# Kernel tuning notes

Measured on AMD Instinct MI355X. Metric: run time of the kernel, lower is better.

The kernel has to match this reference:

```python
import jax, jax.numpy as jnp
import numpy as np

B, S, DIM = 2, 4096, 768
G = DIM // 3          # gate_dim = 256
H, DK = 4, G // 4     # heads=4, d_k=64
SCALE = 1.0 / np.sqrt(DK)


def setup_inputs() -> dict:
    key = jax.random.key(0)
    ks = jax.random.split(key, 9)
    r = lambda k, shp, s: (jax.random.normal(k, shp, dtype=jnp.float32) * s)
    w_s = 1.0 / np.sqrt(G)
    return {
        "x": r(ks[0], (B, S, DIM), 1.0),
        "wq": r(ks[1], (G, G), w_s), "bq": r(ks[2], (G,), 0.01),
        "wk": r(ks[3], (G, G), w_s), "bk": r(ks[4], (G,), 0.01),
        "wv": r(ks[5], (G, G), w_s), "bv": r(ks[6], (G,), 0.01),
        "wo": r(ks[7], (G, G), w_s), "bo": r(ks[8], (G,), 0.01),
    }


def reference(x, wq, bq, wk, bk, wv, bv, wo, bo):
    # chunk(3, dim=-1): q/k/v slices of width G
    xq, xk, xv = x[..., :G], x[..., G:2 * G], x[..., 2 * G:3 * G]
    # linear projections then split into heads: [b, s, h, d]
    q = (xq @ wq.T + bq).reshape(B, S, H, DK)
    k = (xk @ wk.T + bk).reshape(B, S, H, DK)
    v = (xv @ wv.T + bv).reshape(B, S, H, DK)
    scores = jnp.einsum('bihd,bjhd->bijh', q, k) * SCALE  # [b, i, j, h]
    # NOTE: original applies Softmax(dim=1) -> over the QUERY axis i
    attn = jax.nn.softmax(scores, axis=1)
    out = jnp.einsum('bijh,bjhd->bihd', attn, v).reshape(B, S, G)
    return out @ wo.T + bo
```

## Files before the change

kernel.cpp:

```cpp
#include <hip/hip_runtime.h>

#define SEQ   4096
#define HH    4
#define SCALE 0.125f
#define SC2   0.18033688011112042f
#define C16   -23.083120654223414f

typedef __bf16 bf16x8 __attribute__((ext_vector_type(8)));
typedef __bf16 bf16x4 __attribute__((ext_vector_type(4)));
typedef float  f32x4  __attribute__((ext_vector_type(4)));

constexpr size_t OFF_W16  = 0;
constexpr size_t OFF_A    = 131072;
constexpr size_t OFF_AO   = 294912;
constexpr size_t OFF_X16  = 9732096;
constexpr size_t OFF_Q16  = 12877824;
constexpr size_t K16OFF   = 2097152;
constexpr size_t V16OFF   = 4194304;
constexpr size_t OFF_PZ   = 16023552;

__device__ __forceinline__ f32x4 mf(bf16x8 a, bf16x8 b, f32x4 c) {
    return __builtin_amdgcn_mfma_f32_16x16x32_bf16(a, b, c, 0, 0, 0);
}

__device__ __forceinline__ void gload16(const __bf16* g, __bf16* l) {
    __builtin_amdgcn_global_load_lds(
        (const __attribute__((address_space(1))) unsigned int*)g,
        (__attribute__((address_space(3))) unsigned int*)l, 16, 0, 0);
}

__device__ __forceinline__ float ex2(float x) {
    return __builtin_amdgcn_exp2f(x);
}

__global__ void k_prep(const float* __restrict__ x,
                       const float* __restrict__ wq, const float* __restrict__ wk,
                       const float* __restrict__ wv, const float* __restrict__ wo,
                       float* __restrict__ ws) {
    int bx = blockIdx.x, t = threadIdx.x;
    if (bx < 6144) {
        size_t i4 = ((size_t)bx * 256 + t) * 4;
        float4 v = *(const float4*)(x + i4);
        bf16x4 o = {(__bf16)v.x, (__bf16)v.y, (__bf16)v.z, (__bf16)v.w};
        *(bf16x4*)((__bf16*)(ws + OFF_X16) + i4) = o;
    } else if (bx < 6400) {
        int q = bx - 6144;
        int y = q >> 6;
        const float* src = (y == 0) ? wq : (y == 1) ? wk : (y == 2) ? wv : wo;
        float sc = (y == 0) ? SC2 : 1.0f;
        size_t i4 = ((size_t)(q & 63) * 256 + t) * 4;
        float4 v = *(const float4*)(src + i4);
        bf16x4 o = {(__bf16)(v.x * sc), (__bf16)(v.y * sc),
                    (__bf16)(v.z * sc), (__bf16)(v.w * sc)};
        *(bf16x4*)((__bf16*)(ws + OFF_W16) + (size_t)y * 65536 + i4) = o;
    } else {
        size_t i4 = ((size_t)(bx - 6400) * 256 + t) * 4;
        *(float4*)(ws + OFF_AO + i4) = make_float4(0.f, 0.f, 0.f, 0.f);
    }
}

__global__ __launch_bounds__(256) void k_qkv_mfma(const float* __restrict__ bq,
                                                  const float* __restrict__ bk,
                                                  const float* __restrict__ bv,
                                                  float* __restrict__ ws) {
    __shared__ __bf16 sbuf[4][2][1024];
    int t = threadIdx.x, lane = t & 63, w = t >> 6;
    int yw = blockIdx.y;
    int ntb = blockIdx.z * 8;
    int row0 = blockIdx.x * 64 + w * 16;
    int mrow = lane & 15, quad = lane >> 4;
    const __bf16* X16 = (const __bf16*)(ws + OFF_X16);
    const __bf16* W16 = (const __bf16*)(ws + OFF_W16) + (size_t)yw * 65536;
    const float* bias = (yw == 0) ? bq : (yw == 1) ? bk : bv;
    __bf16* Qb = (__bf16*)(ws + OFF_Q16);
    f32x4 acc[8];
#pragma unroll
    for (int n = 0; n < 8; n++) acc[n] = {0.f, 0.f, 0.f, 0.f};
    const __bf16* ap = X16 + (size_t)(row0 + mrow) * 768 + yw * 256 + quad * 8;
    const __bf16* bp = W16 + (size_t)ntb * 4096 + (size_t)mrow * 256 + quad * 8;
    for (int kc = 0; kc < 256; kc += 32) {
        bf16x8 a = *(const bf16x8*)(ap + kc);
#pragma unroll
        for (int nt = 0; nt < 8; nt++) {
            bf16x8 b = *(const bf16x8*)(bp + (size_t)nt * 4096 + kc);
            acc[nt] = mf(a, b, acc[nt]);
        }
    }
    int T = blockIdx.x * 4 + w;
    int b_ = T >> 8, Ts = T & 255;
    int th = Ts & 1;
#pragma unroll
    for (int nt = 0; nt < 8; nt++) {
        int hsel = nt >> 2, c4 = nt & 3;
        int n = (ntb + nt) * 16 + mrow;
        float bb = bias[n];
        if (yw == 0) bb *= SC2;
        __bf16* sb = &sbuf[w][hsel][0];
#pragma unroll
        for (int r = 0; r < 4; r++) {
            float val = acc[nt][r] + bb;
            int loff;
            if (yw == 0) {
                int q2 = ((c4 & 1) << 1) | (mrow >> 3);
                loff = (c4 >> 1) * 512 + (q2 * 16 + quad * 4 + r) * 8 + (mrow & 7);
            } else if (yw == 1) {
                int q2 = ((c4 & 1) << 1) | (mrow >> 3);
                int piece = ((quad & 1) * 2 + (c4 >> 1)) * 4 + q2;
                loff = piece * 64 + ((quad >> 1) * 4 + r) * 8 + (mrow & 7);
            } else {
                loff = c4 * 256 + (quad >> 1) * 128 + mrow * 8 + (quad & 1) * 4 + r;
            }
            sb[loff] = (__bf16)val;
        }
    }
#pragma unroll
    for (int hsel = 0; hsel < 2; hsel++) {
        int h = blockIdx.z * 2 + hsel;
        int bh = b_ * HH + h;
        const __bf16* sb = &sbuf[w][hsel][0];
#pragma unroll
        for (int rd = 0; rd < 2; rd++) {
            int g = rd * 64 + lane;
            bf16x8 vv = *(const bf16x8*)(sb + g * 8);
            size_t gaddr;
            if (yw == 0) {
                gaddr = (((size_t)bh * 256 + Ts) * 2) * 512 + (size_t)g * 8;
            } else if (yw == 1) {
                int p = g >> 3;
                gaddr = K16OFF + (((size_t)bh * 128 + (Ts >> 1)) * 4 + (p >> 2)) * 512
                        + (size_t)((p & 3) * 128 + th * 64 + (g & 7) * 8);
            } else {
                int p = g >> 4;
                gaddr = V16OFF + (((size_t)bh * 128 + (Ts >> 1)) * 4 + (p >> 1)) * 512
                        + (size_t)((th * 2 + (p & 1)) * 128 + (g & 15) * 8);
            }
            *(bf16x8*)(Qb + gaddr) = vv;
        }
    }
}

__global__ __launch_bounds__(256) void k_colstats(float* __restrict__ ws) {
    __shared__ __bf16 qbuf[2][4096];
    int t = threadIdx.x, lane = t & 63, w = t >> 6;
    int jb = blockIdx.x, iy = blockIdx.y, bh = blockIdx.z;
    int jc0 = jb * 8 + w * 2;
    const __bf16* Qp = (const __bf16*)(ws + OFF_Q16);
    const __bf16* Kp = Qp + K16OFF;
    const __bf16* kb = Kp + ((size_t)(bh * 128 + jc0) * 4) * 512 + lane * 8;
    bf16x8 kA0 = *(const bf16x8*)(kb);
    bf16x8 kA1 = *(const bf16x8*)(kb + 512);
    bf16x8 kB0 = *(const bf16x8*)(kb + 1024);
    bf16x8 kB1 = *(const bf16x8*)(kb + 1536);
    bf16x8 kC0 = *(const bf16x8*)(kb + 2048);
    bf16x8 kC1 = *(const bf16x8*)(kb + 2560);
    bf16x8 kD0 = *(const bf16x8*)(kb + 3072);
    bf16x8 kD1 = *(const bf16x8*)(kb + 3584);
    const __bf16* q0 = Qp + ((size_t)(bh * 256 + iy * 16) * 2) * 512 +
                       w * 1024 + lane * 8;
    gload16(q0, qbuf[0] + w * 1024);
    gload16(q0 + 512, qbuf[0] + w * 1024 + 512);
    __syncthreads();
    const f32x4 cin = {C16, C16, C16, C16};
    float z0 = 0.f, z1 = 0.f, z2 = 0.f, z3 = 0.f;
    for (int ic = 0; ic < 4; ic++) {
        const __bf16* cur = qbuf[ic & 1];
        if (ic < 3) {
            const __bf16* qn = Qp + ((size_t)(bh * 256 + iy * 16 + (ic + 1) * 4) * 2) * 512 +
                               w * 1024 + lane * 8;
            gload16(qn, qbuf[(ic + 1) & 1] + w * 1024);
            gload16(qn + 512, qbuf[(ic + 1) & 1] + w * 1024 + 512);
        }
#pragma unroll
        for (int it = 0; it < 4; it++) {
            bf16x8 a0 = *(const bf16x8*)(cur + it * 1024 + lane * 8);
            bf16x8 a1 = *(const bf16x8*)(cur + it * 1024 + 512 + lane * 8);
            f32x4 cA = mf(a0, kA0, cin); cA = mf(a1, kA1, cA);
            f32x4 cB = mf(a0, kB0, cin); cB = mf(a1, kB1, cB);
            f32x4 cC = mf(a0, kC0, cin); cC = mf(a1, kC1, cC);
            f32x4 cD = mf(a0, kD0, cin); cD = mf(a1, kD1, cD);
#pragma unroll
            for (int r = 0; r < 4; r++) {
                z0 += ex2(cA[r]);
                z1 += ex2(cB[r]);
                z2 += ex2(cC[r]);
                z3 += ex2(cD[r]);
            }
        }
        __syncthreads();
    }
    z0 += __shfl_xor(z0, 16, 64);
    z0 += __shfl_xor(z0, 32, 64);
    z1 += __shfl_xor(z1, 16, 64);
    z1 += __shfl_xor(z1, 32, 64);
    z2 += __shfl_xor(z2, 16, 64);
    z2 += __shfl_xor(z2, 32, 64);
    z3 += __shfl_xor(z3, 16, 64);
    z3 += __shfl_xor(z3, 32, 64);
    if (lane < 16) {
        size_t o = OFF_PZ + (size_t)iy * 32768 + (size_t)bh * SEQ +
                   jc0 * 32 + ((lane >> 2) << 3) + (lane & 3);
        ws[o] = z0;
        ws[o + 4] = z1;
        ws[o + 32] = z2;
        ws[o + 36] = z3;
    }
}

__global__ void k_afin(float* __restrict__ ws) {
    int idx = blockIdx.x * 256 + threadIdx.x;
    const float* pz = ws + OFF_PZ;
    float Z = 0.f;
#pragma unroll
    for (int y = 0; y < 16; y++) Z += pz[(size_t)y * 32768 + idx];
    ws[OFF_A + idx] = C16 - __log2f(Z);
}

__global__ __launch_bounds__(256) void k_attnpv(float* __restrict__ ws) {
    __shared__ __align__(16) char pool[28672];
    float* sA = (float*)(pool + 24576);
    int t = threadIdx.x, lane = t & 63, w = t >> 6;
    int jy = blockIdx.y, bh = blockIdx.z;
    int itp = blockIdx.x * 4 + w;
    int it0 = itp * 2;
    int mrow = lane & 15, quad = lane >> 4;
    const __bf16* Qp = (const __bf16*)(ws + OFF_Q16);
    const __bf16* Kp = Qp + K16OFF;
    const __bf16* Vp = Qp + V16OFF;

    {
        const float* Ag = ws + OFF_A + (size_t)bh * SEQ + jy * 1024;
        *(float4*)(sA + t * 4) = *(const float4*)(Ag + t * 4);
    }
    const __bf16* qb = Qp + ((size_t)(bh * 256 + it0) * 2) * 512 + lane * 8;
    bf16x8 aq00 = *(const bf16x8*)(qb);
    bf16x8 aq01 = *(const bf16x8*)(qb + 512);
    bf16x8 aq10 = *(const bf16x8*)(qb + 1024);
    bf16x8 aq11 = *(const bf16x8*)(qb + 1536);

    f32x4 oT0[4], oT1[4];
#pragma unroll
    for (int nd = 0; nd < 4; nd++) {
        oT0[nd] = {0.f, 0.f, 0.f, 0.f};
        oT1[nd] = {0.f, 0.f, 0.f, 0.f};
    }
    int c0g = jy * 32;
    const __bf16* kg = Kp + ((size_t)(bh * 128 + c0g) * 4) * 512 + w * 512 + lane * 8;
    const __bf16* vg = Vp + ((size_t)(bh * 128 + c0g) * 4) * 512 + w * 512 + lane * 8;
    gload16(kg, (__bf16*)pool + w * 512);
    gload16(vg, (__bf16*)(pool + 4096) + w * 512);
    kg += 2048; vg += 2048;
    __syncthreads();

    int bc = 0;
    for (int jt = 0; jt < 32; ++jt) {
        int bn = (bc == 2) ? 0 : bc + 1;
        if (jt < 31) {
            gload16(kg, (__bf16*)(pool + bn * 8192) + w * 512);
            gload16(vg, (__bf16*)(pool + bn * 8192 + 4096) + w * 512);
            kg += 2048; vg += 2048;
            asm volatile("s_waitcnt vmcnt(2)" ::: "memory");
        } else {
            asm volatile("s_waitcnt vmcnt(0)" ::: "memory");
        }
        __builtin_amdgcn_s_barrier();
        const __bf16* curK = (const __bf16*)(pool + bc * 8192);
        const __bf16* curV = (const __bf16*)(pool + bc * 8192 + 4096);
        f32x4 aL = *(const f32x4*)(sA + jt * 32 + quad * 8);
        f32x4 aH = *(const f32x4*)(sA + jt * 32 + quad * 8 + 4);
        bf16x8 ck0 = *(const bf16x8*)(curK + lane * 8);
        bf16x8 ck1 = *(const bf16x8*)(curK + 512 + lane * 8);
        bf16x8 ck2 = *(const bf16x8*)(curK + 1024 + lane * 8);
        bf16x8 ck3 = *(const bf16x8*)(curK + 1536 + lane * 8);
        __builtin_amdgcn_s_setprio(1);
        f32x4 c00 = mf(ck0, aq00, aL); c00 = mf(ck1, aq01, c00);
        f32x4 c01 = mf(ck2, aq00, aH); c01 = mf(ck3, aq01, c01);
        f32x4 c10 = mf(ck0, aq10, aL); c10 = mf(ck1, aq11, c10);
        f32x4 c11 = mf(ck2, aq10, aH); c11 = mf(ck3, aq11, c11);
        __builtin_amdgcn_s_setprio(0);
        bf16x8 pb0, pb1;
#pragma unroll
        for (int r = 0; r < 4; r++) {
            pb0[r]     = (__bf16)ex2(c00[r]);
            pb0[4 + r] = (__bf16)ex2(c01[r]);
            pb1[r]     = (__bf16)ex2(c10[r]);
            pb1[4 + r] = (__bf16)ex2(c11[r]);
        }
        __builtin_amdgcn_s_setprio(1);
#pragma unroll
        for (int nd = 0; nd < 4; nd++) {
            bf16x8 bv = *(const bf16x8*)(curV + nd * 512 + lane * 8);
            oT0[nd] = mf(bv, pb0, oT0[nd]);
            oT1[nd] = mf(bv, pb1, oT1[nd]);
        }
        __builtin_amdgcn_s_setprio(0);
        bc = bn;
    }
    __syncthreads();

    float* sO = (float*)pool + (size_t)w * 1040;
    int b = bh >> 2, h = bh & 3;
    float* AO = ws + OFF_AO;
    int i0 = it0 * 16;
#pragma unroll
    for (int nd = 0; nd < 4; nd++)
#pragma unroll
        for (int r = 0; r < 4; r++)
            sO[mrow * 65 + nd * 16 + quad * 4 + r] = oT0[nd][r];
#pragma unroll
    for (int c = 0; c < 16; c++)
        atomicAdd(&AO[((size_t)(b * SEQ + i0 + c)) * 256 + h * 64 + lane],
                  sO[c * 65 + lane]);
#pragma unroll
    for (int nd = 0; nd < 4; nd++)
#pragma unroll
        for (int r = 0; r < 4; r++)
            sO[mrow * 65 + nd * 16 + quad * 4 + r] = oT1[nd][r];
#pragma unroll
    for (int c = 0; c < 16; c++)
        atomicAdd(&AO[((size_t)(b * SEQ + i0 + 16 + c)) * 256 + h * 64 + lane],
                  sO[c * 65 + lane]);
}

__global__ __launch_bounds__(256) void k_outproj_mfma(const float* __restrict__ bo,
                                                      float* __restrict__ ws,
                                                      float* __restrict__ out) {
    int t = threadIdx.x, lane = t & 63, w = t >> 6;
    int row0 = blockIdx.x * 64 + w * 16;
    int ntb = blockIdx.y * 4;
    int mrow = lane & 15, quad = lane >> 4;
    const float* AO = ws + OFF_AO;
    const __bf16* W16 = (const __bf16*)(ws + OFF_W16) + (size_t)3 * 65536;
    f32x4 acc[4];
#pragma unroll
    for (int n = 0; n < 4; n++) acc[n] = {0.f, 0.f, 0.f, 0.f};
    const float* ap = AO + (size_t)(row0 + mrow) * 256 + quad * 8;
    const __bf16* bp = W16 + (size_t)ntb * 4096 + (size_t)mrow * 256 + quad * 8;
    for (int kc = 0; kc < 256; kc += 32) {
        float4 u = *(const float4*)(ap + kc);
        float4 v = *(const float4*)(ap + kc + 4);
        bf16x8 a = {(__bf16)u.x, (__bf16)u.y, (__bf16)u.z, (__bf16)u.w,
                    (__bf16)v.x, (__bf16)v.y, (__bf16)v.z, (__bf16)v.w};
#pragma unroll
        for (int nt = 0; nt < 4; nt++) {
            bf16x8 b = *(const bf16x8*)(bp + (size_t)nt * 4096 + kc);
            acc[nt] = mf(a, b, acc[nt]);
        }
    }
#pragma unroll
    for (int nt = 0; nt < 4; nt++) {
        int n = (ntb + nt) * 16 + mrow;
        float bb = bo[n];
#pragma unroll
        for (int r = 0; r < 4; r++) {
            int sg = row0 + quad * 4 + r;
            out[(size_t)sg * 256 + n] = acc[nt][r] + bb;
        }
    }
}

extern "C" void kernel_launch(void* const* d_in, const int* in_sizes, int n_in,
                              void* d_out, int out_size, void* d_ws, size_t ws_size,
                              hipStream_t stream) {
    const float* x  = (const float*)d_in[0];
    const float* wq = (const float*)d_in[1];
    const float* bq = (const float*)d_in[2];
    const float* wk = (const float*)d_in[3];
    const float* bk = (const float*)d_in[4];
    const float* wv = (const float*)d_in[5];
    const float* bv = (const float*)d_in[6];
    const float* wo = (const float*)d_in[7];
    const float* bo = (const float*)d_in[8];
    float* ws = (float*)d_ws;
    float* out = (float*)d_out;

    k_prep<<<8448, 256, 0, stream>>>(x, wq, wk, wv, wo, ws);
    k_qkv_mfma<<<dim3(128, 3, 2), 256, 0, stream>>>(bq, bk, bv, ws);
    k_colstats<<<dim3(16, 16, 8), 256, 0, stream>>>(ws);
    k_afin<<<128, 256, 0, stream>>>(ws);
    k_attnpv<<<dim3(32, 4, 8), 256, 0, stream>>>(ws);
    k_outproj_mfma<<<dim3(128, 4), 256, 0, stream>>>(bo, ws, out);
}
```

Before: 198.8 us.

## Fuse column-sum finalize into atomics and triple-buffer colstats Q loads

Drops the k_afin launch: colstats blocks now atomically add their partial column sums straight into the A buffer, which k_prep zeroes first. The log2 finalize moves into k_attnpv's prologue. The colstats Q staging changes from double buffering with two loads per stage to a three-slot ring with one load per stage. It waits on vmcnt explicitly before a raw barrier and raises wave priority around the MFMA block. This removes one kernel launch and the partial-sum round trip through memory, at the cost of 16-way atomic contention per element and nondeterministic float summation order.

```diff
diff --git a/kernel.cpp b/kernel.cpp
--- a/kernel.cpp
+++ b/kernel.cpp
@@ -17,7 +17,6 @@
 constexpr size_t OFF_Q16  = 12877824;
 constexpr size_t K16OFF   = 2097152;
 constexpr size_t V16OFF   = 4194304;
-constexpr size_t OFF_PZ   = 16023552;
 
 __device__ __forceinline__ f32x4 mf(bf16x8 a, bf16x8 b, f32x4 c) {
     return __builtin_amdgcn_mfma_f32_16x16x32_bf16(a, b, c, 0, 0, 0);
@@ -53,9 +52,12 @@
         bf16x4 o = {(__bf16)(v.x * sc), (__bf16)(v.y * sc),
                     (__bf16)(v.z * sc), (__bf16)(v.w * sc)};
         *(bf16x4*)((__bf16*)(ws + OFF_W16) + (size_t)y * 65536 + i4) = o;
-    } else {
+    } else if (bx < 8448) {
         size_t i4 = ((size_t)(bx - 6400) * 256 + t) * 4;
         *(float4*)(ws + OFF_AO + i4) = make_float4(0.f, 0.f, 0.f, 0.f);
+    } else {
+        size_t i4 = ((size_t)(bx - 8448) * 256 + t) * 4;
+        *(float4*)(ws + OFF_A + i4) = make_float4(0.f, 0.f, 0.f, 0.f);
     }
 }
 
@@ -140,7 +142,7 @@
 }
 
 __global__ __launch_bounds__(256) void k_colstats(float* __restrict__ ws) {
-    __shared__ __bf16 qbuf[2][4096];
+    __shared__ __bf16 qbuf[3][2048];
     int t = threadIdx.x, lane = t & 63, w = t >> 6;
     int jb = blockIdx.x, iy = blockIdx.y, bh = blockIdx.z;
     int jc0 = jb * 8 + w * 2;
@@ -155,29 +157,35 @@
     bf16x8 kC1 = *(const bf16x8*)(kb + 2560);
     bf16x8 kD0 = *(const bf16x8*)(kb + 3072);
     bf16x8 kD1 = *(const bf16x8*)(kb + 3584);
-    const __bf16* q0 = Qp + ((size_t)(bh * 256 + iy * 16) * 2) * 512 +
-                       w * 1024 + lane * 8;
-    gload16(q0, qbuf[0] + w * 1024);
-    gload16(q0 + 512, qbuf[0] + w * 1024 + 512);
+    const __bf16* qg = Qp + ((size_t)(bh * 256 + iy * 16) * 2) * 512 +
+                       w * 512 + lane * 8;
+    gload16(qg, qbuf[0] + w * 512);
+    qg += 2048;
     __syncthreads();
     const f32x4 cin = {C16, C16, C16, C16};
     float z0 = 0.f, z1 = 0.f, z2 = 0.f, z3 = 0.f;
-    for (int ic = 0; ic < 4; ic++) {
-        const __bf16* cur = qbuf[ic & 1];
-        if (ic < 3) {
-            const __bf16* qn = Qp + ((size_t)(bh * 256 + iy * 16 + (ic + 1) * 4) * 2) * 512 +
-                               w * 1024 + lane * 8;
-            gload16(qn, qbuf[(ic + 1) & 1] + w * 1024);
-            gload16(qn + 512, qbuf[(ic + 1) & 1] + w * 1024 + 512);
-        }
-#pragma unroll
-        for (int it = 0; it < 4; it++) {
+    int bc = 0;
+    for (int ic = 0; ic < 8; ic++) {
+        int bn = (bc == 2) ? 0 : bc + 1;
+        if (ic < 7) {
+            gload16(qg, qbuf[bn] + w * 512);
+            qg += 2048;
+            asm volatile("s_waitcnt vmcnt(1)" ::: "memory");
+        } else {
+            asm volatile("s_waitcnt vmcnt(0)" ::: "memory");
+        }
+        __builtin_amdgcn_s_barrier();
+        const __bf16* cur = qbuf[bc];
+#pragma unroll
+        for (int it = 0; it < 2; it++) {
             bf16x8 a0 = *(const bf16x8*)(cur + it * 1024 + lane * 8);
             bf16x8 a1 = *(const bf16x8*)(cur + it * 1024 + 512 + lane * 8);
+            __builtin_amdgcn_s_setprio(1);
             f32x4 cA = mf(a0, kA0, cin); cA = mf(a1, kA1, cA);
             f32x4 cB = mf(a0, kB0, cin); cB = mf(a1, kB1, cB);
             f32x4 cC = mf(a0, kC0, cin); cC = mf(a1, kC1, cC);
             f32x4 cD = mf(a0, kD0, cin); cD = mf(a1, kD1, cD);
+            __builtin_amdgcn_s_setprio(0);
 #pragma unroll
             for (int r = 0; r < 4; r++) {
                 z0 += ex2(cA[r]);
@@ -186,7 +194,7 @@
                 z3 += ex2(cD[r]);
             }
         }
-        __syncthreads();
+        bc = bn;
     }
     z0 += __shfl_xor(z0, 16, 64);
     z0 += __shfl_xor(z0, 32, 64);
@@ -197,22 +205,13 @@
     z3 += __shfl_xor(z3, 16, 64);
     z3 += __shfl_xor(z3, 32, 64);
     if (lane < 16) {
-        size_t o = OFF_PZ + (size_t)iy * 32768 + (size_t)bh * SEQ +
-                   jc0 * 32 + ((lane >> 2) << 3) + (lane & 3);
-        ws[o] = z0;
-        ws[o + 4] = z1;
-        ws[o + 32] = z2;
-        ws[o + 36] = z3;
-    }
-}
-
-__global__ void k_afin(float* __restrict__ ws) {
-    int idx = blockIdx.x * 256 + threadIdx.x;
-    const float* pz = ws + OFF_PZ;
-    float Z = 0.f;
-#pragma unroll
-    for (int y = 0; y < 16; y++) Z += pz[(size_t)y * 32768 + idx];
-    ws[OFF_A + idx] = C16 - __log2f(Z);
+        float* Zp = ws + OFF_A + (size_t)bh * SEQ +
+                    jc0 * 32 + ((lane >> 2) << 3) + (lane & 3);
+        atomicAdd(Zp, z0);
+        atomicAdd(Zp + 4, z1);
+        atomicAdd(Zp + 32, z2);
+        atomicAdd(Zp + 36, z3);
+    }
 }
 
 __global__ __launch_bounds__(256) void k_attnpv(float* __restrict__ ws) {
@@ -228,8 +227,11 @@
     const __bf16* Vp = Qp + V16OFF;
 
     {
-        const float* Ag = ws + OFF_A + (size_t)bh * SEQ + jy * 1024;
-        *(float4*)(sA + t * 4) = *(const float4*)(Ag + t * 4);
+        const float* Zg = ws + OFF_A + (size_t)bh * SEQ + jy * 1024;
+        float4 zv = *(const float4*)(Zg + t * 4);
+        float4 av = make_float4(C16 - __log2f(zv.x), C16 - __log2f(zv.y),
+                                C16 - __log2f(zv.z), C16 - __log2f(zv.w));
+        *(float4*)(sA + t * 4) = av;
     }
     const __bf16* qb = Qp + ((size_t)(bh * 256 + it0) * 2) * 512 + lane * 8;
     bf16x8 aq00 = *(const bf16x8*)(qb);
@@ -373,10 +375,9 @@
     float* ws = (float*)d_ws;
     float* out = (float*)d_out;
 
-    k_prep<<<8448, 256, 0, stream>>>(x, wq, wk, wv, wo, ws);
+    k_prep<<<8480, 256, 0, stream>>>(x, wq, wk, wv, wo, ws);
     k_qkv_mfma<<<dim3(128, 3, 2), 256, 0, stream>>>(bq, bk, bv, ws);
     k_colstats<<<dim3(16, 16, 8), 256, 0, stream>>>(ws);
-    k_afin<<<128, 256, 0, stream>>>(ws);
     k_attnpv<<<dim3(32, 4, 8), 256, 0, stream>>>(ws);
     k_outproj_mfma<<<dim3(128, 4), 256, 0, stream>>>(bo, ws, out);
 }
```

New measurement: 198.3 us. About the same (-0.3%).
